# Kernel tuning notes

Hardware: AMD Instinct MI355X
Metric: run time of the kernel (lower is better)

## Reference

```python
import jax, jax.numpy as jnp
import numpy as np

B, N, C = 2, 20000, 256
TEST_MAX_BOX = 5000
IOU_THRESHOLDS = (0.4, 0.6, 0.8)
N_HIDDEN_LAYERS = 6  # six Conv1d(256,256,k=1)+LeakyReLU blocks in mask_w_layers


def setup_inputs() -> dict:
    key = jax.random.key(0)
    ks = jax.random.split(key, 8)
    # valid xyxy boxes: top-left in [0,900), w/h in [4,84)
    xy = jax.random.uniform(ks[0], (B, 2, N), dtype=jnp.float32) * 900.0
    wh = jax.random.uniform(ks[1], (B, 2, N), dtype=jnp.float32) * 80.0 + 4.0
    box = jnp.concatenate([xy, xy + wh], axis=1)              # [B,4,N]
    score = jax.random.uniform(ks[2], (B, 1, N), dtype=jnp.float32)
    feat = jax.random.normal(ks[3], (B, C, N), dtype=jnp.float32)
    W = jax.random.normal(ks[4], (N_HIDDEN_LAYERS, C, C), dtype=jnp.float32) * 0.02
    b = jnp.zeros((N_HIDDEN_LAYERS, C), dtype=jnp.float32)
    Wf = jax.random.normal(ks[5], (len(IOU_THRESHOLDS), C), dtype=jnp.float32) * 0.02
    bf = jnp.zeros((len(IOU_THRESHOLDS),), dtype=jnp.float32)
    return {"box": box, "score": score, "feat": feat, "W": W, "b": b, "Wf": Wf, "bf": bf}


def _box_iou(a, bxs):
    # a: [N,4], bxs: [M,4], xyxy -> [N,M] (torchvision ops.box_iou)
    area_a = (a[:, 2] - a[:, 0]) * (a[:, 3] - a[:, 1])
    area_b = (bxs[:, 2] - bxs[:, 0]) * (bxs[:, 3] - bxs[:, 1])
    lt = jnp.maximum(a[:, None, :2], bxs[None, :, :2])
    rb = jnp.minimum(a[:, None, 2:], bxs[None, :, 2:])
    wh = jnp.clip(rb - lt, 0.0)
    inter = wh[..., 0] * wh[..., 1]
    return inter / (area_a[:, None] + area_b[None, :] - inter)


def reference(box, score, feat, W, b, Wf, bf):
    # forward_test path of LMM
    boxT = jnp.swapaxes(box, 1, 2)                 # [B,N,4]
    s = jnp.swapaxes(score, 1, 2)[..., 0]          # [B,N]
    top_s, keep = jax.lax.top_k(s, TEST_MAX_BOX)   # [B,K] each, sorted desc
    boxK = jnp.take_along_axis(boxT, keep[..., None], axis=1)   # [B,K,4]
    featK = jnp.take_along_axis(feat, keep[:, None, :], axis=2)  # [B,C,K]

    iou = jax.vmap(_box_iou)(boxK, boxK)           # [B,K,K]
    idx = jnp.arange(TEST_MAX_BOX)
    masks = []
    for thr in IOU_THRESHOLDS:
        adjc = jnp.where(iou >= thr, 1.0, 0.0) * top_s[:, :, None]  # [B,K,K]
        max_idx = jnp.argmax(adjc, axis=1)                           # [B,K]
        masks.append((max_idx == idx[None, :]).astype(featK.dtype))
    masks = jnp.stack(masks, axis=1)               # [B,3,K]

    x = featK
    for l in range(N_HIDDEN_LAYERS):
        x = jax.nn.leaky_relu(jnp.einsum('oi,bik->bok', W[l], x) + b[l][:, None], 0.2)
    mask_w = jax.nn.softmax(jnp.einsum('oi,bik->bok', Wf, x) + bf[:, None], axis=1)  # [B,3,K]

    loc_max = jnp.sum(masks * mask_w, axis=1, keepdims=True)  # [B,1,K]
    return (loc_max, keep)
```

## Files before the change

kernel.cpp:

```cpp
#include <hip/hip_runtime.h>

#define B_  2
#define N_  20000
#define C_  256
#define K_  5000
#define M_  (B_ * K_)
#define CAP_ 5376
#define NBIN_ 2048
#define AST_ 264

typedef __attribute__((ext_vector_type(8))) short bf16x8;
typedef __attribute__((ext_vector_type(4))) float f32x4;

__device__ __forceinline__ unsigned short f2bf(float x) {
  unsigned u = __float_as_uint(x);
  return (unsigned short)((u + 0x7fffu + ((u >> 16) & 1u)) >> 16);
}
__device__ __forceinline__ unsigned fkey(float f) {
  unsigned u = __float_as_uint(f);
  return (u & 0x80000000u) ? ~u : (u | 0x80000000u);
}
__device__ __forceinline__ int binof(float s) {
  int b = (int)(s * 2048.0f);
  return b < 0 ? 0 : (b > 2047 ? 2047 : b);
}
__device__ __forceinline__ bf16x8 as_bf(uint4 v) {
  union { uint4 u; bf16x8 b; } c; c.u = v; return c.b;
}

__global__ __launch_bounds__(256) void k_prep(const float* __restrict__ W,
                                              const float* __restrict__ score,
                                              unsigned short* __restrict__ Whi,
                                              int* __restrict__ selb,
                                              int* __restrict__ h_glob,
                                              int* __restrict__ rnk) {
  const int u = blockIdx.x;
  const int t = threadIdx.x;
  if (u >= 192) {
    if (u >= 194) {
      const int i = (u - 194) * 256 + t;
      if (i < B_ * N_) rnk[i] = K_;
      return;
    }
    const int b = u - 192;
    __shared__ int h[NBIN_];
    __shared__ int chs[256];
    const float* s = score + b * N_;
    for (int i = t; i < NBIN_; i += 256) h[i] = 0;
    __syncthreads();
    for (int i = t; i < N_ / 4; i += 256) {
      const float4 v = ((const float4*)s)[i];
      atomicAdd(&h[binof(v.x)], 1);
      atomicAdd(&h[binof(v.y)], 1);
      atomicAdd(&h[binof(v.z)], 1);
      atomicAdd(&h[binof(v.w)], 1);
    }
    __syncthreads();
    int sum = 0;
#pragma unroll
    for (int j = 0; j < 8; ++j) sum += h[t * 8 + j];
    chs[t] = sum;
    __syncthreads();
    for (int off = 1; off < 256; off <<= 1) {
      int v = chs[t] + ((t + off < 256) ? chs[t + off] : 0);
      __syncthreads();
      chs[t] = v;
      __syncthreads();
    }
    const int above = (t + 1 < 256) ? chs[t + 1] : 0;
    if (above < K_ && K_ <= chs[t]) {
      int acc = above;
      for (int i = 7; i >= 0; --i) {
        const int bin = t * 8 + i;
        if (acc + h[bin] >= K_) { selb[b] = bin; break; }
        acc += h[bin];
      }
    }
    for (int i = t; i < NBIN_; i += 256) h_glob[b * NBIN_ + i] = h[i];
    return;
  }
  const int idx = u * 256 + t;
  const int lane = idx & 63;
  const int oi = (idx >> 6) & 1;
  const int ks = (idx >> 7) & 7;
  const int w = (idx >> 10) & 7;
  const int l = idx >> 13;
  const int o = w * 32 + oi * 16 + (lane & 15);
  const int k0 = ks * 32 + (lane >> 4) * 8;
  const float* src = W + ((size_t)(l * C_ + o)) * C_ + k0;
  float4 w0 = *(const float4*)&src[0];
  float4 w1 = *(const float4*)&src[4];
  const float wv[8] = {w0.x, w0.y, w0.z, w0.w, w1.x, w1.y, w1.z, w1.w};
  unsigned short hs[8];
#pragma unroll
  for (int q = 0; q < 8; ++q) hs[q] = f2bf(wv[q]);
  *(uint4*)&Whi[(size_t)idx * 8] = *(const uint4*)&hs[0];
}

__global__ __launch_bounds__(1024) void k_rankscatter(
    const float* __restrict__ score, const int* __restrict__ selb,
    const int* __restrict__ h_glob, const float* __restrict__ box,
    int* __restrict__ keep_i, float* __restrict__ out_keep,
    int* __restrict__ rnk, float* __restrict__ boxK,
    unsigned* __restrict__ maxiou) {
  __shared__ int h[NBIN_];
  __shared__ int sfx[NBIN_];
  __shared__ int chs[1024];
  __shared__ unsigned long long sorted[CAP_];
  const int b = blockIdx.x;
  const int t = threadIdx.x;
  const int selB = selb[b];
  h[t] = h_glob[b * NBIN_ + t];
  h[t + 1024] = h_glob[b * NBIN_ + t + 1024];
  __syncthreads();
  chs[t] = h[2 * t] + h[2 * t + 1];
  __syncthreads();
  for (int off = 1; off < 1024; off <<= 1) {
    int v = chs[t] + ((t + off < 1024) ? chs[t + off] : 0);
    __syncthreads();
    chs[t] = v;
    __syncthreads();
  }
  const int above = (t + 1 < 1024) ? chs[t + 1] : 0;
  sfx[2 * t + 1] = above;
  sfx[2 * t] = above + h[2 * t + 1];
  __syncthreads();
  int S = sfx[selB] + h[selB];
  if (S > CAP_) S = CAP_;
  __syncthreads();
  h[t] = 0; h[t + 1024] = 0;
  __syncthreads();
  const float* s = score + b * N_;
  for (int i4 = t; i4 < N_ / 4; i4 += 1024) {
    const float4 v = ((const float4*)s)[i4];
    const float sv[4] = {v.x, v.y, v.z, v.w};
#pragma unroll
    for (int q = 0; q < 4; ++q) {
      const int bin = binof(sv[q]);
      if (bin >= selB) {
        const int pos = sfx[bin] + atomicAdd(&h[bin], 1);
        if (pos < CAP_) {
          const int n = i4 * 4 + q;
          sorted[pos] = ((unsigned long long)fkey(sv[q]) << 32) |
                        (unsigned)(N_ - 1 - n);
        }
      }
    }
  }
  __syncthreads();
  const float* bb = box + (size_t)b * 4 * N_;
  for (int p = t; p < S; p += 1024) {
    const unsigned long long k = sorted[p];
    const unsigned fk = (unsigned)(k >> 32);
    const unsigned uu = (fk & 0x80000000u) ? (fk & 0x7fffffffu) : ~fk;
    const int bin = binof(__uint_as_float(uu));
    const int start = sfx[bin];
    int end = start + h[bin];
    if (end > S) end = S;
    int c = start;
    for (int q2 = start; q2 < end; ++q2) c += (int)(sorted[q2] > k);
    if (c >= K_) continue;
    const int n = N_ - 1 - (int)(k & 0xffffffffu);
    keep_i[b * K_ + c] = n;
    out_keep[b * K_ + c] = (float)n;
    rnk[b * N_ + n] = c;
    float4 v;
    v.x = bb[n]; v.y = bb[N_ + n]; v.z = bb[2 * N_ + n]; v.w = bb[3 * N_ + n];
    ((float4*)boxK)[b * K_ + c] = v;
    maxiou[b * K_ + c] = 0u;
  }
}

__global__ __launch_bounds__(256) void k_ioug(const float* __restrict__ boxK,
                                              unsigned* __restrict__ maxiou,
                                              const int* __restrict__ rnk,
                                              const float* __restrict__ feat,
                                              unsigned short* __restrict__ Xhi) {
  __shared__ __align__(16) char arena[16640];
  const int u = blockIdx.x;
  const int t = threadIdx.x;
  if (u < 420) {
    const int b = u / 210;
    const int p = u % 210;
    int jt = 0;
    while ((jt + 1) * (jt + 2) / 2 <= p) ++jt;
    const int it = p - jt * (jt + 1) / 2;
    float* sx0 = (float*)arena;
    float* sy0 = sx0 + 256; float* sx1 = sy0 + 256;
    float* sy1 = sx1 + 256; float* sa = sy1 + 256;
    const int gi0 = it * 256;
    const int gl = gi0 + t;
    if (gl < K_) {
      float4 v = ((const float4*)boxK)[b * K_ + gl];
      sx0[t] = v.x; sy0[t] = v.y; sx1[t] = v.z; sy1[t] = v.w;
      sa[t] = __fmul_rn(__fsub_rn(v.z, v.x), __fsub_rn(v.w, v.y));
    } else {
      sx0[t] = 1e30f; sy0[t] = 1e30f; sx1[t] = -1e30f; sy1[t] = -1e30f;
      sa[t] = 0.f;
    }
    __syncthreads();
    const int j = jt * 256 + t;
    if (j >= K_) return;
    float4 v = ((const float4*)boxK)[b * K_ + j];
    const float aj = __fmul_rn(__fsub_rn(v.z, v.x), __fsub_rn(v.w, v.y));
    float mx = 0.f;
    int lim = j - gi0;
    if (lim > 256) lim = 256;
    for (int ii = 0; ii < lim; ++ii) {
      float ltx = fmaxf(sx0[ii], v.x);
      float lty = fmaxf(sy0[ii], v.y);
      float rbx = fminf(sx1[ii], v.z);
      float rby = fminf(sy1[ii], v.w);
      float wx = fmaxf(__fsub_rn(rbx, ltx), 0.f);
      float wy = fmaxf(__fsub_rn(rby, lty), 0.f);
      float inter = __fmul_rn(wx, wy);
      if (inter > 0.f) {
        float uni = __fsub_rn(__fadd_rn(sa[ii], aj), inter);
        mx = fmaxf(mx, __fdiv_rn(inter, uni));
      }
    }
    if (mx > 0.f) atomicMax(&maxiou[b * K_ + j], __float_as_uint(mx));
  } else {
    const int v2 = u - 420;
    const int b = v2 / 1252;
    const int rem = v2 % 1252;
    const int c0 = (rem / 313) * 64;
    const int n0 = (rem % 313) * 64;
    float* T = (float*)arena;
    const int nl = t & 63, wq = t >> 6;
#pragma unroll
    for (int r = 0; r < 16; ++r) {
      const int cl = r * 4 + wq;
      const int n = n0 + nl;
      T[nl * 65 + cl] =
          (n < N_) ? feat[((size_t)(b * C_ + c0 + cl)) * N_ + n] : 0.f;
    }
    __syncthreads();
    const int nn = n0 + (t >> 2);
    if (nn >= N_) return;
    const int r = rnk[b * N_ + nn];
    if (r >= K_) return;
    const int cseg = (t & 3) * 16;
    unsigned short hb[16];
#pragma unroll
    for (int i = 0; i < 16; ++i)
      hb[i] = f2bf(T[(t >> 2) * 65 + cseg + i]);
    const size_t base = (size_t)(b * K_ + r) * C_ + c0 + cseg;
    *(uint4*)&Xhi[base] = *(const uint4*)&hb[0];
    *(uint4*)&Xhi[base + 8] = *(const uint4*)&hb[8];
  }
}

__global__ __launch_bounds__(512, 2) void k_mlp6(
    const unsigned short* __restrict__ Whi,
    const float* __restrict__ bias, const float* __restrict__ Wf,
    const float* __restrict__ bf, const unsigned* __restrict__ maxiou,
    const unsigned short* __restrict__ Xhi,
    float* __restrict__ out_loc) {
  __shared__ __align__(16) unsigned short act_hi[32 * AST_];
  __shared__ float swf[768];
  const int t = threadIdx.x;
  const int m0 = blockIdx.x * 32;

  {
    const int r = t >> 4;
    const int cs = (t & 15) * 16;
    const size_t g = (size_t)(m0 + r) * C_ + cs;
    *(uint4*)&act_hi[r * AST_ + cs] = *(const uint4*)&Xhi[g];
    *(uint4*)&act_hi[r * AST_ + cs + 8] = *(const uint4*)&Xhi[g + 8];
  }
  for (int i = t; i < 768; i += 512) swf[i] = Wf[i];
  __syncthreads();

  const int lane = t & 63;
  const int w = t >> 6;
  const int quad = lane >> 4, l15 = lane & 15;

  for (int l = 0; l < 6; ++l) {
    const size_t wbase = (size_t)(l * 8 + w) * 8192 + (size_t)lane * 8;
    f32x4 acc[2][2];
#pragma unroll
    for (int oi = 0; oi < 2; ++oi)
#pragma unroll
      for (int mi = 0; mi < 2; ++mi) acc[oi][mi] = (f32x4)0.f;
    uint4 nwh[2];
#pragma unroll
    for (int oi = 0; oi < 2; ++oi)
      nwh[oi] = *(const uint4*)&Whi[wbase + oi * 512];
#pragma unroll
    for (int ks = 0; ks < 8; ++ks) {
      bf16x8 wh[2];
#pragma unroll
      for (int oi = 0; oi < 2; ++oi) wh[oi] = as_bf(nwh[oi]);
      if (ks < 7) {
        const size_t nb = wbase + (size_t)(ks + 1) * 1024;
#pragma unroll
        for (int oi = 0; oi < 2; ++oi)
          nwh[oi] = *(const uint4*)&Whi[nb + oi * 512];
      }
      bf16x8 Ah[2];
#pragma unroll
      for (int mi = 0; mi < 2; ++mi)
        Ah[mi] = *(const bf16x8*)&act_hi[(mi * 16 + l15) * AST_ + ks * 32 + quad * 8];
#pragma unroll
      for (int mi = 0; mi < 2; ++mi)
#pragma unroll
        for (int oi = 0; oi < 2; ++oi)
          acc[oi][mi] = __builtin_amdgcn_mfma_f32_16x16x32_bf16(wh[oi], Ah[mi], acc[oi][mi], 0, 0, 0);
    }
    __syncthreads();
    const int o0 = w * 32 + quad * 4;
#pragma unroll
    for (int oi = 0; oi < 2; ++oi) {
      const float4 bb = *(const float4*)&bias[l * C_ + o0 + oi * 16];
#pragma unroll
      for (int mi = 0; mi < 2; ++mi) {
        float y0 = acc[oi][mi][0] + bb.x; y0 = fmaxf(y0, 0.2f * y0);
        float y1 = acc[oi][mi][1] + bb.y; y1 = fmaxf(y1, 0.2f * y1);
        float y2 = acc[oi][mi][2] + bb.z; y2 = fmaxf(y2, 0.2f * y2);
        float y3 = acc[oi][mi][3] + bb.w; y3 = fmaxf(y3, 0.2f * y3);
        uint2 pk;
        pk.x = (unsigned)f2bf(y0) | ((unsigned)f2bf(y1) << 16);
        pk.y = (unsigned)f2bf(y2) | ((unsigned)f2bf(y3) << 16);
        *(uint2*)&act_hi[(mi * 16 + l15) * AST_ + o0 + oi * 16] = pk;
      }
    }
    __syncthreads();
  }

  const int r = t >> 4;
  const int part = t & 15;
  const int m = m0 + r;
  float a0 = 0.f, a1 = 0.f, a2 = 0.f;
  for (int c = part * 16; c < part * 16 + 16; c += 2) {
    const unsigned hv = *(const unsigned*)&act_hi[r * AST_ + c];
    const float x0 = __uint_as_float((hv & 0xffffu) << 16);
    const float x1 = __uint_as_float(hv & 0xffff0000u);
    a0 += swf[c] * x0 + swf[c + 1] * x1;
    a1 += swf[256 + c] * x0 + swf[256 + c + 1] * x1;
    a2 += swf[512 + c] * x0 + swf[512 + c + 1] * x1;
  }
#pragma unroll
  for (int off = 1; off < 16; off <<= 1) {
    a0 += __shfl_xor(a0, off);
    a1 += __shfl_xor(a1, off);
    a2 += __shfl_xor(a2, off);
  }
  if (part == 0 && m < M_) {
    a0 += bf[0]; a1 += bf[1]; a2 += bf[2];
    const float mxv = fmaxf(a0, fmaxf(a1, a2));
    const float e0 = expf(a0 - mxv);
    const float e1 = expf(a1 - mxv);
    const float e2 = expf(a2 - mxv);
    const float inv = 1.f / (e0 + e1 + e2);
    const float miou = __uint_as_float(maxiou[m]);
    float loc = 0.f;
    if (miou < 0.4f) loc += e0;
    if (miou < 0.6f) loc += e1;
    if (miou < 0.8f) loc += e2;
    out_loc[m] = loc * inv;
  }
}

extern "C" void kernel_launch(void* const* d_in, const int* in_sizes, int n_in,
                              void* d_out, int out_size, void* d_ws, size_t ws_size,
                              hipStream_t stream) {
  const float* box   = (const float*)d_in[0];
  const float* score = (const float*)d_in[1];
  const float* feat  = (const float*)d_in[2];
  const float* W     = (const float*)d_in[3];
  const float* bias  = (const float*)d_in[4];
  const float* Wf    = (const float*)d_in[5];
  const float* bf    = (const float*)d_in[6];

  float* out = (float*)d_out;
  float* out_loc  = out;
  float* out_keep = out + M_;

  char* ws = (char*)d_ws;
  int*            keep_i = (int*)(ws + 0);
  float*          boxK   = (float*)(ws + 40960);
  unsigned*       maxiou = (unsigned*)(ws + 201216);
  unsigned short* Whi    = (unsigned short*)(ws + 241664);
  unsigned short* XtA_hi = (unsigned short*)(ws + 1814528);
  int*                rnk    = (int*)(ws + 12169216);
  int*                h_glob = (int*)(ws + 12329216);
  int*                selb   = (int*)(ws + 12345600);

  k_prep<<<351, 256, 0, stream>>>(W, score, Whi, selb, h_glob, rnk);
  k_rankscatter<<<B_, 1024, 0, stream>>>(score, selb, h_glob, box, keep_i,
                                         out_keep, rnk, boxK, maxiou);
  k_ioug<<<2924, 256, 0, stream>>>(boxK, maxiou, rnk, feat, XtA_hi);
  k_mlp6<<<313, 512, 0, stream>>>(Whi, bias, Wf, bf, maxiou, XtA_hi, out_loc);
}
```

Measured before the change: 178.6 us.

## Split top-k histogram and rank-scatter across many blocks

The single-block-per-batch histogram and the 2-block rank/scatter kernel are replaced. The histogram now runs as 8 partial histograms per batch, and selection happens in two multi-block kernels. k_compact scatters candidates into a global buffer using global atomic counters, and k_rank computes each candidate's exact rank in parallel across 21 blocks. This targets the serial bottleneck of two 1024-thread blocks on a large GPU. In exchange it adds a kernel launch, redundant per-block prefix scans, and global atomics and memory traffic in place of LDS.

```diff
diff --git a/kernel.cpp b/kernel.cpp
--- a/kernel.cpp
+++ b/kernel.cpp
@@ -8,6 +8,7 @@
 #define CAP_ 5376
 #define NBIN_ 2048
 #define AST_ 264
+#define HPB_ 8
 
 typedef __attribute__((ext_vector_type(8))) short bf16x8;
 typedef __attribute__((ext_vector_type(4))) float f32x4;
@@ -28,55 +29,82 @@
   union { uint4 u; bf16x8 b; } c; c.u = v; return c.b;
 }
 
+__device__ __forceinline__ void rank_preamble(const int* __restrict__ hp,
+                                              const int t, int* h, int* sfx,
+                                              int* chs, int* selp) {
+  int hb[8];
+  {
+    int4 a0 = {0, 0, 0, 0}, a1 = {0, 0, 0, 0};
+#pragma unroll
+    for (int p = 0; p < HPB_; ++p) {
+      const int4 v0 = *(const int4*)&hp[p * NBIN_ + t * 8];
+      const int4 v1 = *(const int4*)&hp[p * NBIN_ + t * 8 + 4];
+      a0.x += v0.x; a0.y += v0.y; a0.z += v0.z; a0.w += v0.w;
+      a1.x += v1.x; a1.y += v1.y; a1.z += v1.z; a1.w += v1.w;
+    }
+    hb[0] = a0.x; hb[1] = a0.y; hb[2] = a0.z; hb[3] = a0.w;
+    hb[4] = a1.x; hb[5] = a1.y; hb[6] = a1.z; hb[7] = a1.w;
+    *(int4*)&h[t * 8] = a0;
+    *(int4*)&h[t * 8 + 4] = a1;
+  }
+  chs[t] = hb[0] + hb[1] + hb[2] + hb[3] + hb[4] + hb[5] + hb[6] + hb[7];
+  __syncthreads();
+  for (int off = 1; off < 256; off <<= 1) {
+    int v = chs[t] + ((t + off < 256) ? chs[t + off] : 0);
+    __syncthreads();
+    chs[t] = v;
+    __syncthreads();
+  }
+  const int above = (t + 1 < 256) ? chs[t + 1] : 0;
+  int run = above;
+  sfx[t * 8 + 7] = run;
+#pragma unroll
+  for (int i = 7; i > 0; --i) { run += hb[i]; sfx[t * 8 + i - 1] = run; }
+  if (above < K_ && K_ <= chs[t]) {
+    int acc = above;
+#pragma unroll
+    for (int i = 7; i >= 0; --i) {
+      if (acc + hb[i] >= K_) { *selp = t * 8 + i; break; }
+      acc += hb[i];
+    }
+  }
+  __syncthreads();
+}
+
 __global__ __launch_bounds__(256) void k_prep(const float* __restrict__ W,
                                               const float* __restrict__ score,
                                               unsigned short* __restrict__ Whi,
-                                              int* __restrict__ selb,
-                                              int* __restrict__ h_glob,
-                                              int* __restrict__ rnk) {
+                                              int* __restrict__ rnk,
+                                              int* __restrict__ hpart,
+                                              int* __restrict__ gcnt) {
   const int u = blockIdx.x;
   const int t = threadIdx.x;
   if (u >= 192) {
-    if (u >= 194) {
-      const int i = (u - 194) * 256 + t;
+    if (u < 349) {
+      const int i = (u - 192) * 256 + t;
       if (i < B_ * N_) rnk[i] = K_;
       return;
     }
-    const int b = u - 192;
-    __shared__ int h[NBIN_];
-    __shared__ int chs[256];
-    const float* s = score + b * N_;
-    for (int i = t; i < NBIN_; i += 256) h[i] = 0;
-    __syncthreads();
-    for (int i = t; i < N_ / 4; i += 256) {
-      const float4 v = ((const float4*)s)[i];
-      atomicAdd(&h[binof(v.x)], 1);
-      atomicAdd(&h[binof(v.y)], 1);
-      atomicAdd(&h[binof(v.z)], 1);
-      atomicAdd(&h[binof(v.w)], 1);
-    }
-    __syncthreads();
-    int sum = 0;
-#pragma unroll
-    for (int j = 0; j < 8; ++j) sum += h[t * 8 + j];
-    chs[t] = sum;
-    __syncthreads();
-    for (int off = 1; off < 256; off <<= 1) {
-      int v = chs[t] + ((t + off < 256) ? chs[t + off] : 0);
+    if (u < 365) {
+      const int hb = u - 349;
+      const int b = hb >> 3, seg = hb & 7;
+      __shared__ int lh[NBIN_];
+      for (int i = t; i < NBIN_; i += 256) lh[i] = 0;
       __syncthreads();
-      chs[t] = v;
+      const float4* s4 = (const float4*)(score + b * N_);
+      for (int idx = t; idx < 625; idx += 256) {
+        const float4 v = s4[seg * 625 + idx];
+        atomicAdd(&lh[binof(v.x)], 1);
+        atomicAdd(&lh[binof(v.y)], 1);
+        atomicAdd(&lh[binof(v.z)], 1);
+        atomicAdd(&lh[binof(v.w)], 1);
+      }
       __syncthreads();
-    }
-    const int above = (t + 1 < 256) ? chs[t + 1] : 0;
-    if (above < K_ && K_ <= chs[t]) {
-      int acc = above;
-      for (int i = 7; i >= 0; --i) {
-        const int bin = t * 8 + i;
-        if (acc + h[bin] >= K_) { selb[b] = bin; break; }
-        acc += h[bin];
-      }
-    }
-    for (int i = t; i < NBIN_; i += 256) h_glob[b * NBIN_ + i] = h[i];
+      int* dst = hpart + (size_t)hb * NBIN_;
+      for (int i = t; i < NBIN_; i += 256) dst[i] = lh[i];
+      return;
+    }
+    for (int i = t; i < B_ * NBIN_; i += 256) gcnt[i] = 0;
     return;
   }
   const int idx = u * 256 + t;
@@ -97,78 +125,72 @@
   *(uint4*)&Whi[(size_t)idx * 8] = *(const uint4*)&hs[0];
 }
 
-__global__ __launch_bounds__(1024) void k_rankscatter(
-    const float* __restrict__ score, const int* __restrict__ selb,
-    const int* __restrict__ h_glob, const float* __restrict__ box,
-    int* __restrict__ keep_i, float* __restrict__ out_keep,
-    int* __restrict__ rnk, float* __restrict__ boxK,
-    unsigned* __restrict__ maxiou) {
-  __shared__ int h[NBIN_];
-  __shared__ int sfx[NBIN_];
-  __shared__ int chs[1024];
-  __shared__ unsigned long long sorted[CAP_];
-  const int b = blockIdx.x;
+__global__ __launch_bounds__(256) void k_compact(const float* __restrict__ score,
+                                                 const int* __restrict__ hpart,
+                                                 int* __restrict__ gcnt,
+                                                 unsigned long long* __restrict__ sorted_g) {
+  __shared__ int h[NBIN_], sfx[NBIN_], chs[256];
+  __shared__ int sel_s;
+  const int b = blockIdx.y;
   const int t = threadIdx.x;
-  const int selB = selb[b];
-  h[t] = h_glob[b * NBIN_ + t];
-  h[t + 1024] = h_glob[b * NBIN_ + t + 1024];
-  __syncthreads();
-  chs[t] = h[2 * t] + h[2 * t + 1];
-  __syncthreads();
-  for (int off = 1; off < 1024; off <<= 1) {
-    int v = chs[t] + ((t + off < 1024) ? chs[t + off] : 0);
-    __syncthreads();
-    chs[t] = v;
-    __syncthreads();
-  }
-  const int above = (t + 1 < 1024) ? chs[t + 1] : 0;
-  sfx[2 * t + 1] = above;
-  sfx[2 * t] = above + h[2 * t + 1];
-  __syncthreads();
+  rank_preamble(hpart + (size_t)b * HPB_ * NBIN_, t, h, sfx, chs, &sel_s);
+  const int selB = sel_s;
+  if (t >= 250) return;
+  const int i4 = blockIdx.x * 250 + t;
+  const float4 v = ((const float4*)(score + b * N_))[i4];
+  const float sv[4] = {v.x, v.y, v.z, v.w};
+#pragma unroll
+  for (int q = 0; q < 4; ++q) {
+    const int bin = binof(sv[q]);
+    if (bin >= selB) {
+      const int pos = sfx[bin] + atomicAdd(&gcnt[b * NBIN_ + bin], 1);
+      if (pos < CAP_) {
+        const int n = i4 * 4 + q;
+        sorted_g[(size_t)b * CAP_ + pos] =
+            ((unsigned long long)fkey(sv[q]) << 32) | (unsigned)(N_ - 1 - n);
+      }
+    }
+  }
+}
+
+__global__ __launch_bounds__(256) void k_rank(const int* __restrict__ hpart,
+                                              const unsigned long long* __restrict__ sorted_g,
+                                              const float* __restrict__ box,
+                                              int* __restrict__ keep_i,
+                                              float* __restrict__ out_keep,
+                                              int* __restrict__ rnk,
+                                              float* __restrict__ boxK,
+                                              unsigned* __restrict__ maxiou) {
+  __shared__ int h[NBIN_], sfx[NBIN_], chs[256];
+  __shared__ int sel_s;
+  const int b = blockIdx.y;
+  const int t = threadIdx.x;
+  rank_preamble(hpart + (size_t)b * HPB_ * NBIN_, t, h, sfx, chs, &sel_s);
+  const int selB = sel_s;
   int S = sfx[selB] + h[selB];
   if (S > CAP_) S = CAP_;
-  __syncthreads();
-  h[t] = 0; h[t + 1024] = 0;
-  __syncthreads();
-  const float* s = score + b * N_;
-  for (int i4 = t; i4 < N_ / 4; i4 += 1024) {
-    const float4 v = ((const float4*)s)[i4];
-    const float sv[4] = {v.x, v.y, v.z, v.w};
-#pragma unroll
-    for (int q = 0; q < 4; ++q) {
-      const int bin = binof(sv[q]);
-      if (bin >= selB) {
-        const int pos = sfx[bin] + atomicAdd(&h[bin], 1);
-        if (pos < CAP_) {
-          const int n = i4 * 4 + q;
-          sorted[pos] = ((unsigned long long)fkey(sv[q]) << 32) |
-                        (unsigned)(N_ - 1 - n);
-        }
-      }
-    }
-  }
-  __syncthreads();
+  const int p = blockIdx.x * 256 + t;
+  if (p >= S) return;
+  const unsigned long long* sb = sorted_g + (size_t)b * CAP_;
+  const unsigned long long k = sb[p];
+  const unsigned fk = (unsigned)(k >> 32);
+  const unsigned uu = (fk & 0x80000000u) ? (fk & 0x7fffffffu) : ~fk;
+  const int bin = binof(__uint_as_float(uu));
+  const int start = sfx[bin];
+  int end = start + h[bin];
+  if (end > S) end = S;
+  int c = start;
+  for (int q2 = start; q2 < end; ++q2) c += (int)(sb[q2] > k);
+  if (c >= K_) return;
+  const int n = N_ - 1 - (int)(k & 0xffffffffu);
+  keep_i[b * K_ + c] = n;
+  out_keep[b * K_ + c] = (float)n;
+  rnk[b * N_ + n] = c;
   const float* bb = box + (size_t)b * 4 * N_;
-  for (int p = t; p < S; p += 1024) {
-    const unsigned long long k = sorted[p];
-    const unsigned fk = (unsigned)(k >> 32);
-    const unsigned uu = (fk & 0x80000000u) ? (fk & 0x7fffffffu) : ~fk;
-    const int bin = binof(__uint_as_float(uu));
-    const int start = sfx[bin];
-    int end = start + h[bin];
-    if (end > S) end = S;
-    int c = start;
-    for (int q2 = start; q2 < end; ++q2) c += (int)(sorted[q2] > k);
-    if (c >= K_) continue;
-    const int n = N_ - 1 - (int)(k & 0xffffffffu);
-    keep_i[b * K_ + c] = n;
-    out_keep[b * K_ + c] = (float)n;
-    rnk[b * N_ + n] = c;
-    float4 v;
-    v.x = bb[n]; v.y = bb[N_ + n]; v.z = bb[2 * N_ + n]; v.w = bb[3 * N_ + n];
-    ((float4*)boxK)[b * K_ + c] = v;
-    maxiou[b * K_ + c] = 0u;
-  }
+  float4 v;
+  v.x = bb[n]; v.y = bb[N_ + n]; v.z = bb[2 * N_ + n]; v.w = bb[3 * N_ + n];
+  ((float4*)boxK)[b * K_ + c] = v;
+  maxiou[b * K_ + c] = 0u;
 }
 
 __global__ __launch_bounds__(256) void k_ioug(const float* __restrict__ boxK,
@@ -384,12 +406,14 @@
   unsigned short* Whi    = (unsigned short*)(ws + 241664);
   unsigned short* XtA_hi = (unsigned short*)(ws + 1814528);
   int*                rnk    = (int*)(ws + 12169216);
-  int*                h_glob = (int*)(ws + 12329216);
-  int*                selb   = (int*)(ws + 12345600);
-
-  k_prep<<<351, 256, 0, stream>>>(W, score, Whi, selb, h_glob, rnk);
-  k_rankscatter<<<B_, 1024, 0, stream>>>(score, selb, h_glob, box, keep_i,
-                                         out_keep, rnk, boxK, maxiou);
+  int*                hpart  = (int*)(ws + 12329216);
+  int*                gcnt   = (int*)(ws + 12460288);
+  unsigned long long* sorted_g = (unsigned long long*)(ws + 12476672);
+
+  k_prep<<<366, 256, 0, stream>>>(W, score, Whi, rnk, hpart, gcnt);
+  k_compact<<<dim3(20, B_), 256, 0, stream>>>(score, hpart, gcnt, sorted_g);
+  k_rank<<<dim3(21, B_), 256, 0, stream>>>(hpart, sorted_g, box, keep_i,
+                                           out_keep, rnk, boxK, maxiou);
   k_ioug<<<2924, 256, 0, stream>>>(boxK, maxiou, rnk, feat, XtA_hi);
   k_mlp6<<<313, 512, 0, stream>>>(Whi, bias, Wf, bf, maxiou, XtA_hi, out_loc);
 }
```

After: 157.7 us. 1.13x faster.
